# Optimization experiments

Hardware: AMD Instinct MI355X
Metric: run time of the kernel (lower is better)

The kernel has to match this reference:

```python
import jax, jax.numpy as jnp
import numpy as np
import math

B, C, W = 4, 256, 64
GROUPS = 32
EPS = 1e-6


def setup_inputs() -> dict:
    key = jax.random.key(0)
    ks = jax.random.split(key, 6)
    xavier = math.sqrt(2.0 / (C + C))
    return {
        "x": jax.random.normal(ks[0], (B, C, W, W), dtype=jnp.float32),
        "gn_gamma": jnp.ones((C,), dtype=jnp.float32),
        "gn_beta": jnp.zeros((C,), dtype=jnp.float32),
        "wq": jax.random.normal(ks[1], (C, C), dtype=jnp.float32) * xavier,
        "bq": jnp.zeros((C,), dtype=jnp.float32),
        "wk": jax.random.normal(ks[2], (C, C), dtype=jnp.float32) * xavier,
        "bk": jnp.zeros((C,), dtype=jnp.float32),
        "wv": jax.random.normal(ks[3], (C, C), dtype=jnp.float32) * xavier,
        "bv": jnp.zeros((C,), dtype=jnp.float32),
        "wo": jax.random.normal(ks[4], (C, C), dtype=jnp.float32) * 1e-5,
        "bo": jnp.zeros((C,), dtype=jnp.float32),
    }


def _nin(w, b, t):
    # 1x1 conv via shared weights: [O,C] x [B,C,H,W] -> [B,O,H,W]
    return jnp.einsum('oc,bchw->bohw', w, t) + b[None, :, None, None]


def _group_norm(x, gamma, beta):
    b, c, h, w = x.shape
    xr = x.reshape(b, GROUPS, c // GROUPS, h, w)
    mu = xr.mean(axis=(2, 3, 4), keepdims=True)
    var = xr.var(axis=(2, 3, 4), keepdims=True)
    xn = ((xr - mu) / jnp.sqrt(var + EPS)).reshape(b, c, h, w)
    return xn * gamma[None, :, None, None] + beta[None, :, None, None]


def reference(x, gn_gamma, gn_beta, wq, bq, wk, bk, wv, bv, wo, bo):
    b, c, wdt, _ = x.shape
    n = wdt * wdt  # number of spatial tokens
    h = _group_norm(x, gn_gamma, gn_beta)
    q = _nin(wq, bq, h).reshape(b, c, n)
    k = _nin(wk, bk, h).reshape(b, c, n)
    v = _nin(wv, bv, h).reshape(b, c, n)
    scale = 1.0 / math.sqrt(c)
    scores = jnp.einsum('bcn,bcm->bnm', q, k) * scale  # [B, N, N]
    attn = jax.nn.softmax(scores, axis=-1)
    o = jnp.einsum('bnm,bcm->bcn', attn, v).reshape(b, c, wdt, wdt)
    return x + _nin(wo, bo, o)
```

## Files before the change

kernel.cpp:

```cpp
#include <hip/hip_runtime.h>
#include <math.h>

#define B_      4
#define C_      256
#define NTOK    4096
#define GROUPS_ 32
#define CPG_    8
#define EPS_    1e-6f
#define QSCALE  0.0625f
#define NSEG    4
#define KSEG    (NTOK / NSEG)
#define QB      128

typedef __attribute__((ext_vector_type(8)))  short short8v;
typedef __attribute__((ext_vector_type(4)))  float float4v;
typedef __attribute__((ext_vector_type(16))) float f32x16;
typedef __attribute__((ext_vector_type(4)))  unsigned short ushort4v;
typedef unsigned short ushort_t;

__device__ __forceinline__ ushort_t f2bf(float f) {
  union { float f; unsigned u; } v; v.f = f;
  unsigned r = (v.u + 0x7FFFu + ((v.u >> 16) & 1u)) >> 16;
  return (ushort_t)r;
}
__device__ __forceinline__ float bf2f(ushort_t u) {
  union { unsigned u; float f; } v; v.u = ((unsigned)u) << 16; return v.f;
}
__device__ __forceinline__ unsigned cvtpk(float lo, float hi) {
  unsigned r;
  asm("v_cvt_pk_bf16_f32 %0, %1, %2" : "=v"(r) : "v"(lo), "v"(hi));
  return r;
}

__device__ __forceinline__ float4v mfma16(short8v a, short8v b, float4v c) {
  return __builtin_amdgcn_mfma_f32_16x16x32_bf16(a, b, c, 0, 0, 0);
}
__device__ __forceinline__ f32x16 mfma32(short8v a, short8v b, f32x16 c) {
  return __builtin_amdgcn_mfma_f32_32x32x16_bf16(a, b, c, 0, 0, 0);
}

__device__ __forceinline__ void gld16(const ushort_t* g, ushort_t* l) {
  __builtin_amdgcn_global_load_lds(
      (const __attribute__((address_space(1))) unsigned int*)g,
      (__attribute__((address_space(3))) unsigned int*)l, 16, 0, 0);
}

__global__ __launch_bounds__(256) void gn_stats(const float* __restrict__ x,
                                                float* __restrict__ stats) {
  const int bg = blockIdx.x;
  const size_t base = (size_t)bg * CPG_ * NTOK;
  const int t = threadIdx.x;
  float s = 0.f, s2 = 0.f;
  for (int i = t * 4; i < CPG_ * NTOK; i += 1024) {
    float4 v = *reinterpret_cast<const float4*>(x + base + i);
    s  += v.x + v.y + v.z + v.w;
    s2 += v.x * v.x + v.y * v.y + v.z * v.z + v.w * v.w;
  }
  #pragma unroll
  for (int m = 32; m >= 1; m >>= 1) { s += __shfl_xor(s, m); s2 += __shfl_xor(s2, m); }
  __shared__ float red[8];
  const int wv = t >> 6;
  if ((t & 63) == 0) { red[wv] = s; red[4 + wv] = s2; }
  __syncthreads();
  if (t == 0) {
    float ts  = red[0] + red[1] + red[2] + red[3];
    float ts2 = red[4] + red[5] + red[6] + red[7];
    const float inv_n = 1.0f / (float)(CPG_ * NTOK);
    float mu  = ts * inv_n;
    float var = ts2 * inv_n - mu * mu;
    stats[bg * 2]     = mu;
    stats[bg * 2 + 1] = rsqrtf(var + EPS_);
  }
}

__global__ __launch_bounds__(256) void gn_apply(
    const float* __restrict__ x, const float* __restrict__ gamma,
    const float* __restrict__ beta, const float* __restrict__ stats,
    ushort_t* __restrict__ Ht) {
  const int b  = blockIdx.y;
  const int n0 = blockIdx.x * 64;
  const int t  = threadIdx.x;
  __shared__ __align__(16) ushort_t Hs[64][264];
  const float* xb = x + (size_t)b * C_ * NTOK;
  #pragma unroll
  for (int it = 0; it < 16; ++it) {
    const int idx = t + 256 * it;
    const int c   = idx >> 4;
    const int ch  = (idx & 15) * 4;
    float4 v = *reinterpret_cast<const float4*>(xb + (size_t)c * NTOK + n0 + ch);
    const float mu = stats[(b * GROUPS_ + (c >> 3)) * 2];
    const float rs = stats[(b * GROUPS_ + (c >> 3)) * 2 + 1];
    const float ga = gamma[c] * rs;
    const float be = beta[c] - mu * ga;
    Hs[ch + 0][c] = f2bf(v.x * ga + be);
    Hs[ch + 1][c] = f2bf(v.y * ga + be);
    Hs[ch + 2][c] = f2bf(v.z * ga + be);
    Hs[ch + 3][c] = f2bf(v.w * ga + be);
  }
  __syncthreads();
  ushort_t* Hb = Ht + (size_t)b * NTOK * C_;
  #pragma unroll
  for (int it = 0; it < 8; ++it) {
    const int idx = t + 256 * it;
    const int row = idx >> 5;
    const int ch  = (idx & 31) * 8;
    *reinterpret_cast<short8v*>(Hb + (size_t)(n0 + row) * C_ + ch) =
        *reinterpret_cast<const short8v*>(&Hs[row][ch]);
  }
}

__global__ __launch_bounds__(256) void wconv(
    const float* __restrict__ wq, const float* __restrict__ wk,
    const float* __restrict__ wv, const float* __restrict__ wo,
    ushort_t* __restrict__ Wb) {
  const int m = blockIdx.y;
  const float* srcs[4] = {wq, wk, wv, wo};
  const float* s = srcs[m];
  const int i = (blockIdx.x * 256 + threadIdx.x) * 4;
  float4 v = *reinterpret_cast<const float4*>(s + i);
  ushort4v o4 = {f2bf(v.x), f2bf(v.y), f2bf(v.z), f2bf(v.w)};
  *reinterpret_cast<ushort4v*>(Wb + (size_t)m * 65536 + i) = o4;
}

__global__ __launch_bounds__(256) void nin_qkv(
    const ushort_t* __restrict__ Wb, const float* __restrict__ bq,
    const float* __restrict__ bk, const float* __restrict__ bv,
    const ushort_t* __restrict__ Hin,
    ushort_t* __restrict__ Qt, ushort_t* __restrict__ Kt,
    ushort_t* __restrict__ Vv) {
  const int b  = blockIdx.y;
  const int n0 = blockIdx.x * 32;
  const int t  = threadIdx.x;
  const int w  = t >> 6, l = t & 63;
  const int lg = l >> 4, ln = l & 15;
  __shared__ __align__(16) ushort_t Hs[32][264];
  const ushort_t* Hb = Hin + (size_t)b * NTOK * C_;
  #pragma unroll
  for (int it = 0; it < 4; ++it) {
    const int idx = t + 256 * it;
    const int row = idx >> 5;
    const int ch  = (idx & 31) * 8;
    *reinterpret_cast<short8v*>(&Hs[row][ch]) =
        *reinterpret_cast<const short8v*>(Hb + (size_t)(n0 + row) * C_ + ch);
  }
  __syncthreads();

  auto gemm = [&](const ushort_t* W, float4v acc[4][2]) {
    #pragma unroll
    for (int mt = 0; mt < 4; ++mt)
      #pragma unroll
      for (int nt = 0; nt < 2; ++nt) acc[mt][nt] = (float4v){0.f, 0.f, 0.f, 0.f};
    const ushort_t* Wrow = W + (size_t)(64 * w + ln) * C_;
    #pragma unroll
    for (int kk = 0; kk < 8; ++kk) {
      short8v af[4], bfr[2];
      #pragma unroll
      for (int mt = 0; mt < 4; ++mt)
        af[mt] = *reinterpret_cast<const short8v*>(Wrow + mt * 16 * C_ + kk * 32 + 8 * lg);
      #pragma unroll
      for (int nt = 0; nt < 2; ++nt)
        bfr[nt] = *reinterpret_cast<const short8v*>(&Hs[nt * 16 + ln][kk * 32 + 8 * lg]);
      #pragma unroll
      for (int mt = 0; mt < 4; ++mt)
        #pragma unroll
        for (int nt = 0; nt < 2; ++nt)
          acc[mt][nt] = mfma16(af[mt], bfr[nt], acc[mt][nt]);
    }
  };

  float4v acc[4][2];
  #pragma unroll
  for (int m = 0; m < 2; ++m) {
    const float* bias = (m == 0) ? bq : bk;
    const float osc = (m == 0) ? QSCALE : 1.0f;
    ushort_t* dst = (m == 0) ? Qt : Kt;
    gemm(Wb + (size_t)m * 65536, acc);
    #pragma unroll
    for (int mt = 0; mt < 4; ++mt) {
      const int mb = 64 * w + mt * 16 + 4 * lg;
      #pragma unroll
      for (int nt = 0; nt < 2; ++nt) {
        const int n = n0 + nt * 16 + ln;
        ushort4v pk;
        #pragma unroll
        for (int r = 0; r < 4; ++r)
          pk[r] = f2bf((acc[mt][nt][r] + bias[mb + r]) * osc);
        *reinterpret_cast<ushort4v*>(dst + ((size_t)b * NTOK + n) * C_ + mb) = pk;
      }
    }
  }
  gemm(Wb + 2 * 65536, acc);
  #pragma unroll
  for (int mt = 0; mt < 4; ++mt) {
    const int mb = 64 * w + mt * 16 + 4 * lg;
    #pragma unroll
    for (int nt = 0; nt < 2; ++nt) {
      const int n = n0 + nt * 16 + ln;
      const int k  = n & 31, kb = n >> 5;
      const int e  = (k & 3) | (((k >> 3) & 1) << 2);
      const int o  = ((k >> 2) & 1) | (((k >> 4) & 1) << 1);
      #pragma unroll
      for (int r = 0; r < 4; ++r) {
        const int c = mb + r;
        const int s = o ^ ((c >> 1) & 3);
        Vv[((size_t)b * (NTOK / 32) + kb) * (C_ * 32) + (size_t)c * 32 + s * 8 + e] =
            f2bf(acc[mt][nt][r] + bv[mb + r]);
      }
    }
  }
}

__global__ __launch_bounds__(256, 2) void flash8(
    const ushort_t* __restrict__ Qt, const ushort_t* __restrict__ Kt,
    const ushort_t* __restrict__ Vg, ushort_t* __restrict__ O0,
    ushort_t* __restrict__ Orest, float2* __restrict__ ml) {
  const int id  = blockIdx.x;
  const int xcd = id & 7, sq = id >> 3;
  const int combo = xcd + 8 * (sq >> 5);
  const int b   = combo & 3;
  const int seg = combo >> 2;
  const int q0  = (sq & 31) * QB;
  const int t = threadIdx.x, w = t >> 6, l = t & 63;
  const int ln = l & 31, hi = l >> 5;

  __shared__ __align__(16) ushort_t Ks[2][32][256];
  __shared__ __align__(16) ushort_t Vs[3][8192];

  const ushort_t* Kb_ = Kt + (size_t)b * NTOK * C_;
  const ushort_t* Vb_ = Vg + (size_t)b * NTOK * C_;

  short8v qf[16];
  {
    const ushort_t* qrow = Qt + ((size_t)b * NTOK + q0 + 32 * w + ln) * C_ + 8 * hi;
    #pragma unroll
    for (int kk = 0; kk < 16; ++kk)
      qf[kk] = *reinterpret_cast<const short8v*>(qrow + 16 * kk);
  }

  f32x16 Oacc[8];
  #pragma unroll
  for (int ct = 0; ct < 8; ++ct)
    #pragma unroll
    for (int r = 0; r < 16; ++r) Oacc[ct][r] = 0.f;
  float m_run = -1e30f, l_run = 0.f;
  short8v pa0 = {}, pa1 = {};
  const int sx = (ln >> 1) & 3;

  const int kbase = seg * KSEG;
  const int NT = KSEG / 32;

  auto STAGE_K = [&](int buf, int k0) {
    #pragma unroll
    for (int j = 0; j < 4; ++j) {
      const int i   = 4 * w + j;
      const int row = 2 * i + (l >> 5);
      const int nn  = (l & 31) ^ (row & 15);
      gld16(Kb_ + (size_t)(k0 + row) * C_ + 8 * nn, &Ks[buf][2 * i][0]);
    }
  };
  auto STAGE_V = [&](int buf, int k0) {
    const ushort_t* vt = Vb_ + (size_t)(k0 >> 5) * (C_ * 32);
    #pragma unroll
    for (int j = 0; j < 4; ++j) {
      const int i = 4 * w + j;
      gld16(vt + i * 512 + 8 * l, &Vs[buf][i * 512]);
    }
  };
  auto PV = [&](int vb) {
    const ushort_t* Vc = &Vs[vb][0];
    __builtin_amdgcn_s_setprio(1);
    #pragma unroll
    for (int ct = 0; ct < 8; ++ct) {
      const int c = 32 * ct + ln;
      const ushort_t* vr = Vc + c * 32;
      short8v v0 = *reinterpret_cast<const short8v*>(vr + 8 * (hi ^ sx));
      short8v v1 = *reinterpret_cast<const short8v*>(vr + 8 * ((2 | hi) ^ sx));
      Oacc[ct] = mfma32(pa0, v0, Oacc[ct]);
      Oacc[ct] = mfma32(pa1, v1, Oacc[ct]);
    }
    __builtin_amdgcn_s_setprio(0);
  };

  STAGE_K(0, kbase);
  STAGE_V(0, kbase);

  for (int it = 0; it < NT; ++it) {
    asm volatile("s_waitcnt vmcnt(4)" ::: "memory");
    __builtin_amdgcn_sched_barrier(0);
    __syncthreads();
    if (it + 1 < NT) {
      const int nxt = kbase + 32 * (it + 1);
      STAGE_K((it + 1) & 1, nxt);
      STAGE_V((it + 1) % 3, nxt);
    }

    f32x16 sA, sB;
    #pragma unroll
    for (int r = 0; r < 16; ++r) { sA[r] = 0.f; sB[r] = 0.f; }
    const ushort_t* Kc = &Ks[it & 1][0][0];
    __builtin_amdgcn_s_setprio(1);
    #pragma unroll
    for (int kk = 0; kk < 16; kk += 2) {
      short8v k0f = *reinterpret_cast<const short8v*>(
          Kc + ln * 256 + 8 * ((2 * kk + hi) ^ (ln & 15)));
      short8v k1f = *reinterpret_cast<const short8v*>(
          Kc + ln * 256 + 8 * ((2 * kk + 2 + hi) ^ (ln & 15)));
      sA = mfma32(k0f, qf[kk], sA);
      sB = mfma32(k1f, qf[kk + 1], sB);
    }
    __builtin_amdgcn_s_setprio(0);
    f32x16 sacc = sA + sB;

    float mx8[8];
    #pragma unroll
    for (int j = 0; j < 8; ++j) mx8[j] = fmaxf(sacc[j], sacc[j + 8]);
    #pragma unroll
    for (int j = 0; j < 4; ++j) mx8[j] = fmaxf(mx8[j], mx8[j + 4]);
    float pmax = fmaxf(fmaxf(mx8[0], mx8[2]), fmaxf(mx8[1], mx8[3]));
    pmax = fmaxf(pmax, __shfl_xor(pmax, 32));
    const bool need = !__all(pmax - m_run <= 8.0f);

    if (it > 0) PV((it + 2) % 3);

    if (need) {
      const float mnew = fmaxf(m_run, pmax);
      const float alpha = __expf(m_run - mnew);
      m_run = mnew;
      l_run *= alpha;
      float av[16];
      #pragma unroll
      for (int r = 0; r < 16; ++r)
        av[r] = __shfl(alpha, (r & 3) + 8 * (r >> 2) + 4 * hi);
      #pragma unroll
      for (int ct = 0; ct < 8; ++ct)
        #pragma unroll
        for (int r = 0; r < 16; ++r) Oacc[ct][r] *= av[r];
    }

    #pragma unroll
    for (int r = 0; r < 16; ++r) sacc[r] = __expf(sacc[r] - m_run);
    float sm8[8];
    #pragma unroll
    for (int j = 0; j < 8; ++j) sm8[j] = sacc[j] + sacc[j + 8];
    #pragma unroll
    for (int j = 0; j < 4; ++j) sm8[j] += sm8[j + 4];
    float ps = (sm8[0] + sm8[2]) + (sm8[1] + sm8[3]);
    ps += __shfl_xor(ps, 32);
    l_run += ps;
    union { unsigned u[4]; short8v v; } P0, P1;
    #pragma unroll
    for (int j = 0; j < 4; ++j) {
      P0.u[j] = cvtpk(sacc[2 * j], sacc[2 * j + 1]);
      P1.u[j] = cvtpk(sacc[8 + 2 * j], sacc[9 + 2 * j]);
    }
    pa0 = P0.v;
    pa1 = P1.v;
  }

  asm volatile("s_waitcnt vmcnt(0)" ::: "memory");
  __builtin_amdgcn_sched_barrier(0);
  __syncthreads();
  PV((NT - 1) % 3);

  ushort_t* Op = (seg == 0 ? O0 : Orest + (size_t)(seg - 1) * (size_t)B_ * NTOK * C_)
               + (size_t)b * NTOK * C_;
  #pragma unroll
  for (int ct = 0; ct < 8; ++ct)
    #pragma unroll
    for (int r = 0; r < 16; ++r) {
      const int qr = q0 + 32 * w + (r & 3) + 8 * (r >> 2) + 4 * hi;
      Op[(size_t)qr * C_ + 32 * ct + ln] = f2bf(Oacc[ct][r]);
    }
  if (hi == 0)
    ml[(seg * B_ + b) * NTOK + q0 + 32 * w + ln] = make_float2(m_run, l_run);
}

__global__ __launch_bounds__(256) void nin_final(
    const ushort_t* __restrict__ Wo, const float* __restrict__ bo,
    const ushort_t* __restrict__ O0, const ushort_t* __restrict__ Orest,
    const float2* __restrict__ ml, const float* __restrict__ xres,
    float* __restrict__ out) {
  const int b  = blockIdx.y;
  const int n0 = blockIdx.x * 32;
  const int t  = threadIdx.x;
  const int w  = t >> 6, l = t & 63;
  const int lg = l >> 4, ln = l & 15;
  __shared__ __align__(16) ushort_t Hs[32][264];
  const size_t SLOT = (size_t)B_ * NTOK * C_;
  #pragma unroll
  for (int it = 0; it < 4; ++it) {
    const int idx = t + 256 * it;
    const int row = idx >> 5;
    const int ch  = (idx & 31) * 8;
    const int n   = n0 + row;
    float m4[NSEG], l4[NSEG], M = -1e30f;
    #pragma unroll
    for (int s = 0; s < NSEG; ++s) {
      float2 v = ml[(s * B_ + b) * NTOK + n];
      m4[s] = v.x; l4[s] = v.y;
      M = fmaxf(M, v.x);
    }
    float L = 0.f, wsc[NSEG];
    #pragma unroll
    for (int s = 0; s < NSEG; ++s) { wsc[s] = __expf(m4[s] - M); L += wsc[s] * l4[s]; }
    const float inv = 1.0f / L;
    float acc8[8];
    #pragma unroll
    for (int j = 0; j < 8; ++j) acc8[j] = 0.f;
    #pragma unroll
    for (int s = 0; s < NSEG; ++s) {
      const ushort_t* op = (s == 0 ? O0 : Orest + (size_t)(s - 1) * SLOT);
      short8v v = *reinterpret_cast<const short8v*>(
          op + ((size_t)b * NTOK + n) * C_ + ch);
      #pragma unroll
      for (int j = 0; j < 8; ++j) acc8[j] += wsc[s] * bf2f((ushort_t)v[j]);
    }
    union { ushort_t us[8]; short8v v; } o8;
    #pragma unroll
    for (int j = 0; j < 8; ++j) o8.us[j] = f2bf(acc8[j] * inv);
    *reinterpret_cast<short8v*>(&Hs[row][ch]) = o8.v;
  }
  __syncthreads();

  float4v acc[4][2];
  #pragma unroll
  for (int mt = 0; mt < 4; ++mt)
    #pragma unroll
    for (int nt = 0; nt < 2; ++nt) acc[mt][nt] = (float4v){0.f, 0.f, 0.f, 0.f};
  const ushort_t* Wrow = Wo + (size_t)(64 * w + ln) * C_;
  #pragma unroll
  for (int kk = 0; kk < 8; ++kk) {
    short8v af[4], bfr[2];
    #pragma unroll
    for (int mt = 0; mt < 4; ++mt)
      af[mt] = *reinterpret_cast<const short8v*>(Wrow + mt * 16 * C_ + kk * 32 + 8 * lg);
    #pragma unroll
    for (int nt = 0; nt < 2; ++nt)
      bfr[nt] = *reinterpret_cast<const short8v*>(&Hs[nt * 16 + ln][kk * 32 + 8 * lg]);
    #pragma unroll
    for (int mt = 0; mt < 4; ++mt)
      #pragma unroll
      for (int nt = 0; nt < 2; ++nt)
        acc[mt][nt] = mfma16(af[mt], bfr[nt], acc[mt][nt]);
  }
  #pragma unroll
  for (int mt = 0; mt < 4; ++mt) {
    const int mb = 64 * w + mt * 16 + 4 * lg;
    #pragma unroll
    for (int nt = 0; nt < 2; ++nt) {
      const int n = n0 + nt * 16 + ln;
      #pragma unroll
      for (int r = 0; r < 4; ++r) {
        const size_t off = ((size_t)b * C_ + mb + r) * NTOK + n;
        out[off] = acc[mt][nt][r] + bo[mb + r] + xres[off];
      }
    }
  }
}

extern "C" void kernel_launch(void* const* d_in, const int* in_sizes, int n_in,
                              void* d_out, int out_size, void* d_ws, size_t ws_size,
                              hipStream_t stream) {
  (void)in_sizes; (void)n_in; (void)out_size; (void)ws_size;
  const float* x     = (const float*)d_in[0];
  const float* gamma = (const float*)d_in[1];
  const float* beta  = (const float*)d_in[2];
  const float* wq    = (const float*)d_in[3];
  const float* bq    = (const float*)d_in[4];
  const float* wk    = (const float*)d_in[5];
  const float* bk    = (const float*)d_in[6];
  const float* wv    = (const float*)d_in[7];
  const float* bv    = (const float*)d_in[8];
  const float* wo    = (const float*)d_in[9];
  const float* bo    = (const float*)d_in[10];
  float* out = (float*)d_out;

  ushort_t* ws16 = (ushort_t*)d_ws;
  const size_t SLOT = (size_t)B_ * NTOK * C_;

  ushort_t* Ht  = ws16;
  ushort_t* Qt  = ws16 + SLOT;
  ushort_t* Kt  = ws16 + 2 * SLOT;
  ushort_t* Vb  = ws16 + 3 * SLOT;
  ushort_t* OpR = ws16 + 4 * SLOT;
  ushort_t* Op0 = Ht;
  ushort_t* Wb  = ws16 + 7 * SLOT;
  float*  stats = (float*)(Wb + 4 * 65536);
  float2* mlp   = (float2*)(stats + 256);

  gn_stats<<<dim3(B_ * GROUPS_), 256, 0, stream>>>(x, stats);
  gn_apply<<<dim3(NTOK / 64, B_), 256, 0, stream>>>(x, gamma, beta, stats, Ht);
  wconv<<<dim3(64, 4), 256, 0, stream>>>(wq, wk, wv, wo, Wb);

  dim3 gg(NTOK / 32, B_);
  nin_qkv<<<gg, 256, 0, stream>>>(Wb, bq, bk, bv, Ht, Qt, Kt, Vb);

  flash8<<<dim3(NSEG * B_ * (NTOK / QB)), 256, 0, stream>>>(Qt, Kt, Vb, Op0, OpR, mlp);

  nin_final<<<gg, 256, 0, stream>>>(Wb + 3 * 65536, bo, Op0, OpR, mlp, x, out);
}
```

Before: 186.3 us.

## Fuse group-norm stats and apply; simplify flash loop to double-buffered PV

Group-norm statistics and normalization now run in one kernel per (batch, group), so the separate stats buffer and one launch go away. The fused kernel writes 8-channel bf16 vectors straight to the token-major buffer instead of transposing through shared memory. The attention kernel drops its three-deep V buffer and deferred PV step, which overlapped PV of the previous tile with QK of the current one. It now uses two V buffers and runs PV in the same iteration after a second barrier. This saves LDS and simplifies the loop but loses that QK/PV overlap, and the fused norm kernel uses only 128 blocks with strided scalar reads.

Result: faster. 165.2 us (-11.3%).

```diff
diff --git a/kernel.cpp b/kernel.cpp
--- a/kernel.cpp
+++ b/kernel.cpp
@@ -45,11 +45,14 @@
       (__attribute__((address_space(3))) unsigned int*)l, 16, 0, 0);
 }
 
-__global__ __launch_bounds__(256) void gn_stats(const float* __restrict__ x,
-                                                float* __restrict__ stats) {
+__global__ __launch_bounds__(256) void gn_fused(
+    const float* __restrict__ x, const float* __restrict__ gamma,
+    const float* __restrict__ beta, ushort_t* __restrict__ Ht) {
   const int bg = blockIdx.x;
+  const int b = bg >> 5, g = bg & 31;
   const size_t base = (size_t)bg * CPG_ * NTOK;
   const int t = threadIdx.x;
+
   float s = 0.f, s2 = 0.f;
   for (int i = t * 4; i < CPG_ * NTOK; i += 1024) {
     float4 v = *reinterpret_cast<const float4*>(x + base + i);
@@ -59,6 +62,7 @@
   #pragma unroll
   for (int m = 32; m >= 1; m >>= 1) { s += __shfl_xor(s, m); s2 += __shfl_xor(s2, m); }
   __shared__ float red[8];
+  __shared__ float stats[2];
   const int wv = t >> 6;
   if ((t & 63) == 0) { red[wv] = s; red[4 + wv] = s2; }
   __syncthreads();
@@ -68,44 +72,27 @@
     const float inv_n = 1.0f / (float)(CPG_ * NTOK);
     float mu  = ts * inv_n;
     float var = ts2 * inv_n - mu * mu;
-    stats[bg * 2]     = mu;
-    stats[bg * 2 + 1] = rsqrtf(var + EPS_);
-  }
-}
-
-__global__ __launch_bounds__(256) void gn_apply(
-    const float* __restrict__ x, const float* __restrict__ gamma,
-    const float* __restrict__ beta, const float* __restrict__ stats,
-    ushort_t* __restrict__ Ht) {
-  const int b  = blockIdx.y;
-  const int n0 = blockIdx.x * 64;
-  const int t  = threadIdx.x;
-  __shared__ __align__(16) ushort_t Hs[64][264];
-  const float* xb = x + (size_t)b * C_ * NTOK;
-  #pragma unroll
-  for (int it = 0; it < 16; ++it) {
-    const int idx = t + 256 * it;
-    const int c   = idx >> 4;
-    const int ch  = (idx & 15) * 4;
-    float4 v = *reinterpret_cast<const float4*>(xb + (size_t)c * NTOK + n0 + ch);
-    const float mu = stats[(b * GROUPS_ + (c >> 3)) * 2];
-    const float rs = stats[(b * GROUPS_ + (c >> 3)) * 2 + 1];
-    const float ga = gamma[c] * rs;
-    const float be = beta[c] - mu * ga;
-    Hs[ch + 0][c] = f2bf(v.x * ga + be);
-    Hs[ch + 1][c] = f2bf(v.y * ga + be);
-    Hs[ch + 2][c] = f2bf(v.z * ga + be);
-    Hs[ch + 3][c] = f2bf(v.w * ga + be);
+    stats[0] = mu;
+    stats[1] = rsqrtf(var + EPS_);
   }
   __syncthreads();
-  ushort_t* Hb = Ht + (size_t)b * NTOK * C_;
-  #pragma unroll
-  for (int it = 0; it < 8; ++it) {
-    const int idx = t + 256 * it;
-    const int row = idx >> 5;
-    const int ch  = (idx & 31) * 8;
-    *reinterpret_cast<short8v*>(Hb + (size_t)(n0 + row) * C_ + ch) =
-        *reinterpret_cast<const short8v*>(&Hs[row][ch]);
+  const float mu = stats[0], rs = stats[1];
+
+  float ga[8], be[8];
+  #pragma unroll
+  for (int c = 0; c < 8; ++c) {
+    ga[c] = gamma[g * 8 + c] * rs;
+    be[c] = beta[g * 8 + c] - mu * ga[c];
+  }
+  ushort_t* Hb = Ht + (size_t)b * NTOK * C_ + g * 8;
+  #pragma unroll
+  for (int it2 = 0; it2 < 16; ++it2) {
+    const int n = t + 256 * it2;
+    union { ushort_t us[8]; short8v v; } o8;
+    #pragma unroll
+    for (int c = 0; c < 8; ++c)
+      o8.us[c] = f2bf(x[base + (size_t)c * NTOK + n] * ga[c] + be[c]);
+    *reinterpret_cast<short8v*>(Hb + (size_t)n * C_) = o8.v;
   }
 }
 
@@ -210,7 +197,7 @@
   }
 }
 
-__global__ __launch_bounds__(256, 2) void flash8(
+__global__ __launch_bounds__(256, 2) void flash9(
     const ushort_t* __restrict__ Qt, const ushort_t* __restrict__ Kt,
     const ushort_t* __restrict__ Vg, ushort_t* __restrict__ O0,
     ushort_t* __restrict__ Orest, float2* __restrict__ ml) {
@@ -224,7 +211,7 @@
   const int ln = l & 31, hi = l >> 5;
 
   __shared__ __align__(16) ushort_t Ks[2][32][256];
-  __shared__ __align__(16) ushort_t Vs[3][8192];
+  __shared__ __align__(16) ushort_t Vs[2][8192];
 
   const ushort_t* Kb_ = Kt + (size_t)b * NTOK * C_;
   const ushort_t* Vb_ = Vg + (size_t)b * NTOK * C_;
@@ -243,8 +230,6 @@
     #pragma unroll
     for (int r = 0; r < 16; ++r) Oacc[ct][r] = 0.f;
   float m_run = -1e30f, l_run = 0.f;
-  short8v pa0 = {}, pa1 = {};
-  const int sx = (ln >> 1) & 3;
 
   const int kbase = seg * KSEG;
   const int NT = KSEG / 32;
@@ -266,8 +251,86 @@
       gld16(vt + i * 512 + 8 * l, &Vs[buf][i * 512]);
     }
   };
-  auto PV = [&](int vb) {
-    const ushort_t* Vc = &Vs[vb][0];
+
+  int cur = 0;
+  STAGE_K(0, kbase);
+  STAGE_V(0, kbase);
+
+  for (int it = 0; it < NT; ++it) {
+    asm volatile("s_waitcnt vmcnt(4)" ::: "memory");
+    __builtin_amdgcn_sched_barrier(0);
+    __syncthreads();
+    const bool pre = (it + 1 < NT);
+    if (pre) {
+      const int nxt = kbase + 32 * (it + 1);
+      STAGE_K(cur ^ 1, nxt);
+      STAGE_V(cur ^ 1, nxt);
+    }
+
+    f32x16 sA, sB;
+    #pragma unroll
+    for (int r = 0; r < 16; ++r) { sA[r] = 0.f; sB[r] = 0.f; }
+    const ushort_t* Kc = &Ks[cur][0][0];
+    __builtin_amdgcn_s_setprio(1);
+    #pragma unroll
+    for (int kk = 0; kk < 16; kk += 2) {
+      short8v k0f = *reinterpret_cast<const short8v*>(
+          Kc + ln * 256 + 8 * ((2 * kk + hi) ^ (ln & 15)));
+      short8v k1f = *reinterpret_cast<const short8v*>(
+          Kc + ln * 256 + 8 * ((2 * kk + 2 + hi) ^ (ln & 15)));
+      sA = mfma32(k0f, qf[kk], sA);
+      sB = mfma32(k1f, qf[kk + 1], sB);
+    }
+    __builtin_amdgcn_s_setprio(0);
+    f32x16 sacc = sA + sB;
+
+    float mx8[8];
+    #pragma unroll
+    for (int j = 0; j < 8; ++j) mx8[j] = fmaxf(sacc[j], sacc[j + 8]);
+    #pragma unroll
+    for (int j = 0; j < 4; ++j) mx8[j] = fmaxf(mx8[j], mx8[j + 4]);
+    float pmax = fmaxf(fmaxf(mx8[0], mx8[2]), fmaxf(mx8[1], mx8[3]));
+    pmax = fmaxf(pmax, __shfl_xor(pmax, 32));
+    if (!__all(pmax - m_run <= 8.0f)) {
+      const float mnew = fmaxf(m_run, pmax);
+      const float alpha = __expf(m_run - mnew);
+      m_run = mnew;
+      l_run *= alpha;
+      float av[16];
+      #pragma unroll
+      for (int r = 0; r < 16; ++r)
+        av[r] = __shfl(alpha, (r & 3) + 8 * (r >> 2) + 4 * hi);
+      #pragma unroll
+      for (int ct = 0; ct < 8; ++ct)
+        #pragma unroll
+        for (int r = 0; r < 16; ++r) Oacc[ct][r] *= av[r];
+    }
+    float sm8[8];
+    #pragma unroll
+    for (int r = 0; r < 16; ++r) sacc[r] = __expf(sacc[r] - m_run);
+    #pragma unroll
+    for (int j = 0; j < 8; ++j) sm8[j] = sacc[j] + sacc[j + 8];
+    #pragma unroll
+    for (int j = 0; j < 4; ++j) sm8[j] += sm8[j + 4];
+    float ps = (sm8[0] + sm8[2]) + (sm8[1] + sm8[3]);
+    ps += __shfl_xor(ps, 32);
+    l_run += ps;
+
+    union { unsigned u[4]; short8v v; } P0, P1;
+    #pragma unroll
+    for (int j = 0; j < 4; ++j) {
+      P0.u[j] = cvtpk(sacc[2 * j], sacc[2 * j + 1]);
+      P1.u[j] = cvtpk(sacc[8 + 2 * j], sacc[9 + 2 * j]);
+    }
+    const short8v pa0 = P0.v, pa1 = P1.v;
+
+    if (pre) asm volatile("s_waitcnt vmcnt(8)" ::: "memory");
+    else     asm volatile("s_waitcnt vmcnt(0)" ::: "memory");
+    __builtin_amdgcn_sched_barrier(0);
+    __syncthreads();
+
+    const ushort_t* Vc = &Vs[cur][0];
+    const int sx = (ln >> 1) & 3;
     __builtin_amdgcn_s_setprio(1);
     #pragma unroll
     for (int ct = 0; ct < 8; ++ct) {
@@ -279,88 +342,8 @@
       Oacc[ct] = mfma32(pa1, v1, Oacc[ct]);
     }
     __builtin_amdgcn_s_setprio(0);
-  };
-
-  STAGE_K(0, kbase);
-  STAGE_V(0, kbase);
-
-  for (int it = 0; it < NT; ++it) {
-    asm volatile("s_waitcnt vmcnt(4)" ::: "memory");
-    __builtin_amdgcn_sched_barrier(0);
-    __syncthreads();
-    if (it + 1 < NT) {
-      const int nxt = kbase + 32 * (it + 1);
-      STAGE_K((it + 1) & 1, nxt);
-      STAGE_V((it + 1) % 3, nxt);
-    }
-
-    f32x16 sA, sB;
-    #pragma unroll
-    for (int r = 0; r < 16; ++r) { sA[r] = 0.f; sB[r] = 0.f; }
-    const ushort_t* Kc = &Ks[it & 1][0][0];
-    __builtin_amdgcn_s_setprio(1);
-    #pragma unroll
-    for (int kk = 0; kk < 16; kk += 2) {
-      short8v k0f = *reinterpret_cast<const short8v*>(
-          Kc + ln * 256 + 8 * ((2 * kk + hi) ^ (ln & 15)));
-      short8v k1f = *reinterpret_cast<const short8v*>(
-          Kc + ln * 256 + 8 * ((2 * kk + 2 + hi) ^ (ln & 15)));
-      sA = mfma32(k0f, qf[kk], sA);
-      sB = mfma32(k1f, qf[kk + 1], sB);
-    }
-    __builtin_amdgcn_s_setprio(0);
-    f32x16 sacc = sA + sB;
-
-    float mx8[8];
-    #pragma unroll
-    for (int j = 0; j < 8; ++j) mx8[j] = fmaxf(sacc[j], sacc[j + 8]);
-    #pragma unroll
-    for (int j = 0; j < 4; ++j) mx8[j] = fmaxf(mx8[j], mx8[j + 4]);
-    float pmax = fmaxf(fmaxf(mx8[0], mx8[2]), fmaxf(mx8[1], mx8[3]));
-    pmax = fmaxf(pmax, __shfl_xor(pmax, 32));
-    const bool need = !__all(pmax - m_run <= 8.0f);
-
-    if (it > 0) PV((it + 2) % 3);
-
-    if (need) {
-      const float mnew = fmaxf(m_run, pmax);
-      const float alpha = __expf(m_run - mnew);
-      m_run = mnew;
-      l_run *= alpha;
-      float av[16];
-      #pragma unroll
-      for (int r = 0; r < 16; ++r)
-        av[r] = __shfl(alpha, (r & 3) + 8 * (r >> 2) + 4 * hi);
-      #pragma unroll
-      for (int ct = 0; ct < 8; ++ct)
-        #pragma unroll
-        for (int r = 0; r < 16; ++r) Oacc[ct][r] *= av[r];
-    }
-
-    #pragma unroll
-    for (int r = 0; r < 16; ++r) sacc[r] = __expf(sacc[r] - m_run);
-    float sm8[8];
-    #pragma unroll
-    for (int j = 0; j < 8; ++j) sm8[j] = sacc[j] + sacc[j + 8];
-    #pragma unroll
-    for (int j = 0; j < 4; ++j) sm8[j] += sm8[j + 4];
-    float ps = (sm8[0] + sm8[2]) + (sm8[1] + sm8[3]);
-    ps += __shfl_xor(ps, 32);
-    l_run += ps;
-    union { unsigned u[4]; short8v v; } P0, P1;
-    #pragma unroll
-    for (int j = 0; j < 4; ++j) {
-      P0.u[j] = cvtpk(sacc[2 * j], sacc[2 * j + 1]);
-      P1.u[j] = cvtpk(sacc[8 + 2 * j], sacc[9 + 2 * j]);
-    }
-    pa0 = P0.v;
-    pa1 = P1.v;
-  }
-
-  asm volatile("s_waitcnt vmcnt(0)" ::: "memory");
-  __builtin_amdgcn_sched_barrier(0);
-  __syncthreads();
-  PV((NT - 1) % 3);
+    cur ^= 1;
+  }
 
   ushort_t* Op = (seg == 0 ? O0 : Orest + (size_t)(seg - 1) * (size_t)B_ * NTOK * C_)
                + (size_t)b * NTOK * C_;
@@ -485,17 +468,16 @@
   ushort_t* OpR = ws16 + 4 * SLOT;
   ushort_t* Op0 = Ht;
   ushort_t* Wb  = ws16 + 7 * SLOT;
-  float*  stats = (float*)(Wb + 4 * 65536);
-  float2* mlp   = (float2*)(stats + 256);
-
-  gn_stats<<<dim3(B_ * GROUPS_), 256, 0, stream>>>(x, stats);
-  gn_apply<<<dim3(NTOK / 64, B_), 256, 0, stream>>>(x, gamma, beta, stats, Ht);
+  float*  extra = (float*)(Wb + 4 * 65536);
+  float2* mlp   = (float2*)(extra + 256);
+
+  gn_fused<<<dim3(B_ * GROUPS_), 256, 0, stream>>>(x, gamma, beta, Ht);
   wconv<<<dim3(64, 4), 256, 0, stream>>>(wq, wk, wv, wo, Wb);
 
   dim3 gg(NTOK / 32, B_);
   nin_qkv<<<gg, 256, 0, stream>>>(Wb, bq, bk, bv, Ht, Qt, Kt, Vb);
 
-  flash8<<<dim3(NSEG * B_ * (NTOK / QB)), 256, 0, stream>>>(Qt, Kt, Vb, Op0, OpR, mlp);
+  flash9<<<dim3(NSEG * B_ * (NTOK / QB)), 256, 0, stream>>>(Qt, Kt, Vb, Op0, OpR, mlp);
 
   nin_final<<<gg, 256, 0, stream>>>(Wb + 3 * 65536, bo, Op0, OpR, mlp, x, out);
 }
```
